# Kernel tuning notes

Measured on AMD Instinct MI355X. Metric: run time of the kernel, lower is better.

## Reference

```python
import jax, jax.numpy as jnp
import numpy as np

N_FLOWS, N_LINKS, L, P, D = 50000, 5000, 8, 80, 16
ITERS = 12
# (mean, scale) applied as (x - mean) * scale, matching the TF code
MS_FIELDS = ['flow_traffic', 'flow_packets', 'flow_pkts_per_burst', 'flow_bitrate_per_burst',
             'flow_packet_size', 'flow_p90PktSize', 'rate', 'flow_ipg_mean', 'ibg',
             'flow_ipg_var', 'link_capacity']
MS = {f: (0.1, 2.0) for f in MS_FIELDS}


def _gru(h, x, Wk, Wr, b):
    # Keras GRUCell (reset_after=True): bias has shape [2, 3D]
    a = x @ Wk + b[0]
    g = h @ Wr + b[1]
    az, ar, ah = jnp.split(a, 3, axis=-1)
    gz, gr, gh = jnp.split(g, 3, axis=-1)
    z = jax.nn.sigmoid(az + gz)
    r = jax.nn.sigmoid(ar + gr)
    return z * h + (1.0 - z) * jnp.tanh(ah + r * gh)


def setup_inputs() -> dict:
    key = jax.random.key(0)
    ks = jax.random.split(key, 48)
    u = lambda i, shape: jax.random.uniform(ks[i], shape, jnp.float32)
    w = lambda i, shape: (jax.random.normal(ks[i], shape, jnp.float32) * 0.3)
    inp = {
        'flow_traffic': u(0, (N_FLOWS, 1)),
        'flow_packets': u(1, (N_FLOWS, 1)),
        'max_link_load': jnp.ones((1, 1), jnp.float32),
        'flow_pkts_per_burst': u(2, (N_FLOWS, 1)),
        'flow_bitrate_per_burst': u(3, (N_FLOWS, 1)),
        'flow_packet_size': u(4, (N_FLOWS, 1)),
        'flow_type': u(5, (N_FLOWS, 2)),
        'flow_ipg_mean': u(6, (N_FLOWS, 1)),
        'ibg': u(7, (N_FLOWS, 1)),
        'flow_p90PktSize': u(8, (N_FLOWS, 1)),
        'rate': u(9, (N_FLOWS, 1)),
        'flow_ipg_var': u(10, (N_FLOWS, 1)),
        'link_capacity': u(11, (N_LINKS, 1)) + 0.5,  # keep capacities away from 0
        # params
        'fe_W1': w(12, (13, D)), 'fe_b1': jnp.zeros((D,), jnp.float32),
        'fe_W2': w(13, (D, D)), 'fe_b2': jnp.zeros((D,), jnp.float32),
        'le_W1': w(14, (3, D)), 'le_b1': jnp.zeros((D,), jnp.float32),
        'le_W2': w(15, (D, D)), 'le_b2': jnp.zeros((D,), jnp.float32),
        'att_W': w(16, (D, D)), 'att_b': jnp.zeros((D,), jnp.float32),
        'pgru_Wk': w(17, (D, 3 * D)), 'pgru_Wr': w(18, (D, 3 * D)),
        'pgru_b': jnp.zeros((2, 3 * D), jnp.float32),
        'lgru_Wk': w(19, (D, 3 * D)), 'lgru_Wr': w(20, (D, 3 * D)),
        'lgru_b': jnp.zeros((2, 3 * D), jnp.float32),
        'ro_W1': w(21, (D, D // 2)), 'ro_b1': jnp.zeros((D // 2,), jnp.float32),
        'ro_W2': w(22, (D // 2, D // 4)), 'ro_b2': jnp.zeros((D // 4,), jnp.float32),
        'ro_W3': w(23, (D // 4, 1)), 'ro_b3': jnp.zeros((1,), jnp.float32),
        # integer graph structure
        'flow_length': jax.random.randint(ks[24], (N_FLOWS,), 0, 1000, jnp.int32),
        'link_to_path': jax.random.randint(ks[25], (N_FLOWS, L), 0, N_LINKS, jnp.int32),
        'path_to_link': jnp.stack([
            jax.random.randint(ks[26], (N_LINKS, P), 0, N_FLOWS, jnp.int32),
            jax.random.randint(ks[27], (N_LINKS, P), 0, L + 1, jnp.int32)], axis=-1),
    }
    return inp


def reference(flow_traffic, flow_packets, max_link_load, flow_pkts_per_burst,
              flow_bitrate_per_burst, flow_packet_size, flow_type, flow_ipg_mean,
              ibg, flow_p90PktSize, rate, flow_ipg_var, link_capacity,
              fe_W1, fe_b1, fe_W2, fe_b2, le_W1, le_b1, le_W2, le_b2,
              att_W, att_b, pgru_Wk, pgru_Wr, pgru_b, lgru_Wk, lgru_Wr, lgru_b,
              ro_W1, ro_b1, ro_W2, ro_b2, ro_W3, ro_b3,
              flow_length, link_to_path, path_to_link):
    nrm = lambda x, f: (x - MS[f][0]) * MS[f][1]
    flow_idx = path_to_link[:, :, 0]   # [M, P]
    pos_idx = path_to_link[:, :, 1]    # [M, P]

    # link load from gathered flow traffic
    path_gather_traffic = flow_traffic[flow_idx]                 # [M, P, 1]
    load = path_gather_traffic.sum(axis=1) / (link_capacity * 1e9)
    normal_load = load / jnp.squeeze(max_link_load)

    flow_feats = jnp.concatenate([
        nrm(flow_traffic, 'flow_traffic'), nrm(flow_packets, 'flow_packets'),
        nrm(ibg, 'ibg'), nrm(rate, 'rate'), nrm(flow_p90PktSize, 'flow_p90PktSize'),
        nrm(flow_packet_size, 'flow_packet_size'),
        nrm(flow_bitrate_per_burst, 'flow_bitrate_per_burst'),
        nrm(flow_ipg_mean, 'flow_ipg_mean'), nrm(flow_ipg_var, 'flow_ipg_var'),
        nrm(flow_pkts_per_burst, 'flow_pkts_per_burst'),
        flow_length.astype(jnp.float32)[:, None], flow_type], axis=1)     # [N, 13]
    path_state = jax.nn.selu(jax.nn.selu(flow_feats @ fe_W1 + fe_b1) @ fe_W2 + fe_b2)

    link_feats = jnp.concatenate([nrm(link_capacity, 'link_capacity'), load, normal_load], axis=1)
    link_state = jax.nn.selu(jax.nn.selu(link_feats @ le_W1 + le_b1) @ le_W2 + le_b2)

    def rnn_step(h, x):
        h2 = _gru(h, x, pgru_Wk, pgru_Wr, pgru_b)
        return h2, h2

    path_state_sequence = None
    for _ in range(ITERS):
        link_gather = link_state[link_to_path]                   # [N, L, D]
        prev_path_state = path_state
        path_state, seq = jax.lax.scan(rnn_step, prev_path_state,
                                       jnp.swapaxes(link_gather, 0, 1))
        seq = jnp.swapaxes(seq, 0, 1)                            # [N, L, D]
        path_state_sequence = jnp.concatenate([prev_path_state[:, None], seq], axis=1)
        path_gather = path_state_sequence[flow_idx, pos_idx]     # [M, P, D]
        att = jax.nn.leaky_relu(path_gather @ att_W + att_b, negative_slope=0.01)
        score = jax.nn.softmax(att, axis=-1)                     # softmax over feature dim (K.softmax default)
        path_sum = (score * path_gather).sum(axis=1)             # [M, D]
        link_state = _gru(link_state, path_sum, lgru_Wk, lgru_Wr, lgru_b)

    h = jax.nn.selu(path_state_sequence[:, 1:] @ ro_W1 + ro_b1)
    h = jax.nn.selu(h @ ro_W2 + ro_b2)
    occupancy = jax.nn.softplus(h @ ro_W3 + ro_b3)               # [N, L, 1]
    capacity_gather = link_capacity[link_to_path]                # [N, L, 1]
    queue_delay = (occupancy / capacity_gather).sum(axis=1)      # [N, 1]
    return queue_delay
```

## Files before the change

kernel.cpp:

```cpp
#include <hip/hip_runtime.h>
#include <hip/hip_bf16.h>

#define N_FLOWS 50000
#define N_LINKS 5000
#define LPATH 8
#define PLINK 80
#define DIM 16
#define ITERS 12

typedef __attribute__((ext_vector_type(4))) float f32x4;
typedef __attribute__((ext_vector_type(8))) short bf16x8;

#define L2E 1.4426950408889634f
#define NL2E (-1.4426950408889634f)
#define P2L2E 2.8853900817779268f

#define SWZ(x, pat) __int_as_float(__builtin_amdgcn_ds_swizzle(__float_as_int(x), (pat)))

template <int CTRL>
__device__ __forceinline__ float dppmov_(float x) {
    return __int_as_float(__builtin_amdgcn_update_dpp(
        0, __float_as_int(x), CTRL, 0xF, 0xF, true));
}
#define ROR1 0x121
#define ROR2 0x122
#define ROR4 0x124
#define ROR8 0x128

__device__ __forceinline__ float rcp_(float x) { return __builtin_amdgcn_rcpf(x); }
__device__ __forceinline__ float exp2_(float x) { return __builtin_amdgcn_exp2f(x); }
__device__ __forceinline__ float sigmoid2_(float s) { return rcp_(1.f + exp2_(s)); }
__device__ __forceinline__ float tanh2_(float s) { return 1.f - 2.f * rcp_(1.f + exp2_(s)); }
__device__ __forceinline__ float selu_(float x) {
    const float sc = 1.0507009873554805f, al = 1.6732632423543772f;
    return x > 0.f ? sc * x : sc * al * expm1f(x);
}
__device__ __forceinline__ float softplus_(float x) {
    return fmaxf(x, 0.f) + log1pf(__expf(-fabsf(x)));
}
__device__ __forceinline__ ushort f2bf_(float x) {
    unsigned u = __float_as_uint(x);
    u += 0x7fffu + ((u >> 16) & 1u);
    return (ushort)(u >> 16);
}
__device__ __forceinline__ float bf2f_(ushort h) {
    return __uint_as_float(((unsigned)h) << 16);
}

__global__ __launch_bounds__(256) void k_prep(
    const float* __restrict__ pWr, const float* __restrict__ attW,
    const float* __restrict__ lWk, const float* __restrict__ lWr,
    const float* __restrict__ pWk,
    ushort* __restrict__ wfrag, float* __restrict__ lWk_t,
    float* __restrict__ lWr_t, float* __restrict__ pWk_t) {
    int i = blockIdx.x * 256 + threadIdx.x;
    if (i < 768) {
        int t = i;
        int j = t / 48, r = t % 48;
        float sc = (r / 16) == 2 ? P2L2E : NL2E;
        lWk_t[t] = lWk[(r % 16) * 48 + (r / 16) * 16 + j] * sc;
    } else if (i < 1536) {
        int t = i - 768;
        int j = t / 48, r = t % 48;
        float sc = (r / 16) == 2 ? P2L2E : NL2E;
        lWr_t[t] = lWr[(r % 16) * 48 + (r / 16) * 16 + j] * sc;
    } else if (i < 2304) {
        int t = i - 1536;
        pWk_t[t] = pWk[(t % 16) * 48 + (t / 16)];
    } else if (i < 6400) {
        int t = i - 2304;
        int frag = t >> 9;
        int s = t & 511;
        int lane = s >> 3;
        int e = s & 7;
        int gate = frag >> 1;
        int isLo = frag & 1;
        int n = lane & 15;
        int k = ((lane >> 4) * 8 + e) & 15;
        float raw;
        if (gate < 3) {
            float sc = gate == 2 ? P2L2E : NL2E;
            raw = pWr[k * 48 + gate * 16 + n] * sc;
        } else {
            raw = attW[k * 16 + n] * L2E;
        }
        ushort hi = f2bf_(raw);
        wfrag[t] = isLo ? f2bf_(raw - bf2f_(hi)) : hi;
    }
}

__global__ __launch_bounds__(256) void k_load(const int* __restrict__ p2l,
                                              const float* __restrict__ flow_traffic,
                                              const float* __restrict__ link_capacity,
                                              float* __restrict__ load) {
    int wave = (blockIdx.x * 256 + threadIdx.x) >> 6;
    int lane = threadIdx.x & 63;
    if (wave >= N_LINKS) return;
    float s = 0.f;
    for (int p = lane; p < PLINK; p += 64) {
        int flow = p2l[(wave * PLINK + p) * 2];
        s += flow_traffic[flow];
    }
#pragma unroll
    for (int off = 32; off; off >>= 1) s += __shfl_xor(s, off, 64);
    if (lane == 0) load[wave] = s / (link_capacity[wave] * 1e9f);
}

__global__ __launch_bounds__(256) void k_flow_init(
    const float* __restrict__ flow_traffic, const float* __restrict__ flow_packets,
    const float* __restrict__ ibg, const float* __restrict__ rate,
    const float* __restrict__ p90, const float* __restrict__ pkt_size,
    const float* __restrict__ bitrate_pb, const float* __restrict__ ipg_mean,
    const float* __restrict__ ipg_var, const float* __restrict__ pkts_pb,
    const int* __restrict__ flow_length, const float* __restrict__ flow_type,
    const float* __restrict__ W1, const float* __restrict__ b1,
    const float* __restrict__ W2, const float* __restrict__ b2,
    float* __restrict__ path_state) {
    int f = blockIdx.x * 256 + threadIdx.x;
    if (f >= N_FLOWS) return;
    float feats[13];
    feats[0] = (flow_traffic[f] - 0.1f) * 2.f;
    feats[1] = (flow_packets[f] - 0.1f) * 2.f;
    feats[2] = (ibg[f] - 0.1f) * 2.f;
    feats[3] = (rate[f] - 0.1f) * 2.f;
    feats[4] = (p90[f] - 0.1f) * 2.f;
    feats[5] = (pkt_size[f] - 0.1f) * 2.f;
    feats[6] = (bitrate_pb[f] - 0.1f) * 2.f;
    feats[7] = (ipg_mean[f] - 0.1f) * 2.f;
    feats[8] = (ipg_var[f] - 0.1f) * 2.f;
    feats[9] = (pkts_pb[f] - 0.1f) * 2.f;
    feats[10] = (float)flow_length[f];
    feats[11] = flow_type[f * 2 + 0];
    feats[12] = flow_type[f * 2 + 1];
    float h1[DIM];
#pragma unroll
    for (int j = 0; j < DIM; ++j) {
        float a = b1[j];
#pragma unroll
        for (int k = 0; k < 13; ++k) a = fmaf(feats[k], W1[k * DIM + j], a);
        h1[j] = selu_(a);
    }
#pragma unroll
    for (int j = 0; j < DIM; ++j) {
        float a = b2[j];
#pragma unroll
        for (int k = 0; k < DIM; ++k) a = fmaf(h1[k], W2[k * DIM + j], a);
        path_state[f * DIM + j] = selu_(a);
    }
}

__global__ __launch_bounds__(256) void k_link_init(
    const float* __restrict__ link_capacity, const float* __restrict__ load,
    const float* __restrict__ max_link_load,
    const float* __restrict__ W1, const float* __restrict__ b1,
    const float* __restrict__ W2, const float* __restrict__ b2,
    const float* __restrict__ pWk, const float* __restrict__ pb,
    float* __restrict__ link_state, float* __restrict__ xform) {
    int l = blockIdx.x * 256 + threadIdx.x;
    if (l >= N_LINKS) return;
    float feats[3];
    feats[0] = (link_capacity[l] - 0.1f) * 2.f;
    feats[1] = load[l];
    feats[2] = load[l] / max_link_load[0];
    float h1[DIM];
#pragma unroll
    for (int j = 0; j < DIM; ++j) {
        float a = b1[j];
#pragma unroll
        for (int k = 0; k < 3; ++k) a = fmaf(feats[k], W1[k * DIM + j], a);
        h1[j] = selu_(a);
    }
    float h2[DIM];
#pragma unroll
    for (int j = 0; j < DIM; ++j) {
        float a = b2[j];
#pragma unroll
        for (int k = 0; k < DIM; ++k) a = fmaf(h1[k], W2[k * DIM + j], a);
        h2[j] = selu_(a);
        link_state[l * DIM + j] = h2[j];
    }
#pragma unroll
    for (int c = 0; c < 3 * DIM; ++c) {
        float a = (c < 32) ? (pb[c] + pb[48 + c]) : pb[c];
#pragma unroll
        for (int k = 0; k < DIM; ++k) a = fmaf(h2[k], pWk[k * 48 + c], a);
        float sc = (c < 32) ? NL2E : P2L2E;
        xform[l * 64 + (c & 15) * 4 + (c >> 4)] = a * sc;
    }
}

template <bool LAST>
__global__ __launch_bounds__(256) void k_flow_pass(
    const int* __restrict__ l2p, const float* __restrict__ xform,
    float* __restrict__ path_state, float* __restrict__ sv,
    const ushort* __restrict__ wfrag, const float* __restrict__ b,
    const float* __restrict__ attB) {
    __shared__ __align__(16) ushort hx[4][16][40];
    __shared__ int lnk[4][16][8];
    int tid = threadIdx.x;
    int wid = tid >> 6, lane = tid & 63;
    int g = lane >> 4, j = lane & 15;
    int fbase = blockIdx.x * 64 + wid * 16;
    {
        int lf = lane >> 2;
        int off = (lane & 3) * 2;
        int fc = fbase + lf; if (fc >= N_FLOWS) fc = N_FLOWS - 1;
        int2 v = *(const int2*)(l2p + fc * LPATH + off);
        *(int2*)&lnk[wid][lf][off] = v;
    }
    bf16x8 WzH = *(const bf16x8*)(wfrag + (0 * 512 + lane * 8));
    bf16x8 WzL = *(const bf16x8*)(wfrag + (1 * 512 + lane * 8));
    bf16x8 WrH = *(const bf16x8*)(wfrag + (2 * 512 + lane * 8));
    bf16x8 WrL = *(const bf16x8*)(wfrag + (3 * 512 + lane * 8));
    bf16x8 WhH = *(const bf16x8*)(wfrag + (4 * 512 + lane * 8));
    bf16x8 WhL = *(const bf16x8*)(wfrag + (5 * 512 + lane * 8));
    bf16x8 WaH = *(const bf16x8*)(wfrag + (6 * 512 + lane * 8));
    bf16x8 WaL = *(const bf16x8*)(wfrag + (7 * 512 + lane * 8));
    float bh = P2L2E * b[80 + j];
    float ab = L2E * attB[j];
    f32x4 bhv = {bh, bh, bh, bh};
    f32x4 abv = {ab, ab, ab, ab};
    f32x4 zero = {0.f, 0.f, 0.f, 0.f};
    int fr[4];
    f32x4 hC;
#pragma unroll
    for (int r = 0; r < 4; ++r) {
        fr[r] = fbase + g * 4 + r;
        int fc = fr[r] < N_FLOWS ? fr[r] : N_FLOWS - 1;
        hC[r] = path_state[fc * DIM + j];
    }
#pragma unroll
    for (int p = 0; p <= LPATH; ++p) {
        bf16x8 A = {};
        if (!LAST || p < LPATH) {
#pragma unroll
            for (int r = 0; r < 4; ++r) {
                ushort hi = f2bf_(hC[r]);
                hx[wid][g * 4 + r][j] = hi;
                hx[wid][g * 4 + r][16 + j] = f2bf_(hC[r] - bf2f_(hi));
            }
            A = *(const bf16x8*)&hx[wid][j][g * 8];
        }
        if constexpr (!LAST) {
            f32x4 att = __builtin_amdgcn_mfma_f32_16x16x32_bf16(A, WaH, abv, 0, 0, 0);
            att = __builtin_amdgcn_mfma_f32_16x16x32_bf16(A, WaL, att, 0, 0, 0);
#pragma unroll
            for (int r = 0; r < 4; ++r) {
                float a = att[r];
                a = a > 0.f ? a : 0.01f * a;
                float m = a;
                m = fmaxf(m, dppmov_<ROR1>(m));
                m = fmaxf(m, dppmov_<ROR2>(m));
                m = fmaxf(m, dppmov_<ROR4>(m));
                m = fmaxf(m, dppmov_<ROR8>(m));
                float e = exp2_(a - m);
                float s = e;
                s += dppmov_<ROR1>(s);
                s += dppmov_<ROR2>(s);
                s += dppmov_<ROR4>(s);
                s += dppmov_<ROR8>(s);
                if (fr[r] < N_FLOWS)
                    sv[p * (N_FLOWS * DIM) + fr[r] * DIM + j] = e * rcp_(s) * hC[r];
            }
        } else {
            if (p > 0) {
#pragma unroll
                for (int r = 0; r < 4; ++r)
                    if (fr[r] < N_FLOWS)
                        sv[p * (N_FLOWS * DIM) + fr[r] * DIM + j] = hC[r];
            }
        }
        if (p < LPATH) {
            f32x4 Gz = __builtin_amdgcn_mfma_f32_16x16x32_bf16(A, WzH, zero, 0, 0, 0);
            Gz = __builtin_amdgcn_mfma_f32_16x16x32_bf16(A, WzL, Gz, 0, 0, 0);
            f32x4 Gr = __builtin_amdgcn_mfma_f32_16x16x32_bf16(A, WrH, zero, 0, 0, 0);
            Gr = __builtin_amdgcn_mfma_f32_16x16x32_bf16(A, WrL, Gr, 0, 0, 0);
            f32x4 Gh = __builtin_amdgcn_mfma_f32_16x16x32_bf16(A, WhH, bhv, 0, 0, 0);
            Gh = __builtin_amdgcn_mfma_f32_16x16x32_bf16(A, WhL, Gh, 0, 0, 0);
#pragma unroll
            for (int r = 0; r < 4; ++r) {
                int link = lnk[wid][g * 4 + r][p];
                f32x4 xq = *(const f32x4*)(xform + link * 64 + j * 4);
                float z = sigmoid2_(xq[0] + Gz[r]);
                float rr = sigmoid2_(xq[1] + Gr[r]);
                float cand = tanh2_(fmaf(rr, Gh[r], xq[2]));
                hC[r] = fmaf(z, hC[r] - cand, cand);
            }
        }
    }
    if constexpr (!LAST) {
#pragma unroll
        for (int r = 0; r < 4; ++r)
            if (fr[r] < N_FLOWS) path_state[fr[r] * DIM + j] = hC[r];
    }
}

__global__ __launch_bounds__(256, 4) void k_link_pass(
    const int* __restrict__ p2l, const float* __restrict__ sv,
    float* __restrict__ link_state,
    const float* __restrict__ lWk_t, const float* __restrict__ lWr_t,
    const float* __restrict__ b,
    const float* __restrict__ pWk_t, const float* __restrict__ pb,
    float* __restrict__ xform) {
    __shared__ float xb_[4][16];
    __shared__ float hb_[4][16];
    int tid = threadIdx.x;
    int li = tid >> 6;
    int lane = tid & 63;
    int sl = lane >> 4, j = lane & 15;
    int link = blockIdx.x * 4 + li;
    float ps = 0.f;
#pragma unroll 4
    for (int i = 0; i < PLINK / 4; ++i) {
        int p = sl + 4 * i;
        int2 fp = ((const int2*)p2l)[link * PLINK + p];
        ps += sv[fp.y * (N_FLOWS * DIM) + fp.x * DIM + j];
    }
    ps += __shfl_xor(ps, 16, 64);
    ps += __shfl_xor(ps, 32, 64);
    float h = link_state[link * DIM + j];
    if (sl == 0) { xb_[li][j] = ps; hb_[li][j] = h; }
    float xv[16], hv[16];
#pragma unroll
    for (int q = 0; q < 4; ++q) {
        f32x4 x4 = ((const f32x4*)xb_[li])[q];
        f32x4 h4 = ((const f32x4*)hb_[li])[q];
#pragma unroll
        for (int e = 0; e < 4; ++e) { xv[q * 4 + e] = x4[e]; hv[q * 4 + e] = h4[e]; }
    }
    float az = NL2E * b[j], ar = NL2E * b[16 + j], ah = P2L2E * b[32 + j];
    float gz = NL2E * b[48 + j], gr = NL2E * b[64 + j], gh = P2L2E * b[80 + j];
    const float* kz = lWk_t + j * 48;
    const float* rz = lWr_t + j * 48;
#pragma unroll
    for (int k = 0; k < 16; ++k) {
        az = fmaf(xv[k], kz[k], az);
        ar = fmaf(xv[k], kz[16 + k], ar);
        ah = fmaf(xv[k], kz[32 + k], ah);
        gz = fmaf(hv[k], rz[k], gz);
        gr = fmaf(hv[k], rz[16 + k], gr);
        gh = fmaf(hv[k], rz[32 + k], gh);
    }
    float z = sigmoid2_(az + gz);
    float r = sigmoid2_(ar + gr);
    float cand = tanh2_(fmaf(r, gh, ah));
    float hn = fmaf(z, h - cand, cand);
    if (sl == 0) {
        link_state[link * DIM + j] = hn;
        hb_[li][j] = hn;
    }
    float nv[16];
#pragma unroll
    for (int q = 0; q < 4; ++q) {
        f32x4 n4 = ((const f32x4*)hb_[li])[q];
#pragma unroll
        for (int e = 0; e < 4; ++e) nv[q * 4 + e] = n4[e];
    }
    int c = lane;
    if (c < 48) {
        const float* pw = pWk_t + c * 16;
        float a = (c < 32) ? (pb[c] + pb[48 + c]) : pb[c];
#pragma unroll
        for (int k = 0; k < 16; ++k) a = fmaf(nv[k], pw[k], a);
        float sc = (c < 32) ? NL2E : P2L2E;
        xform[link * 64 + (c & 15) * 4 + (c >> 4)] = a * sc;
    }
}

__global__ __launch_bounds__(256) void k_readout(
    const float* __restrict__ sv, const int* __restrict__ l2p,
    const float* __restrict__ link_capacity,
    const float* __restrict__ W1, const float* __restrict__ b1,
    const float* __restrict__ W2, const float* __restrict__ b2,
    const float* __restrict__ W3, const float* __restrict__ b3,
    float* __restrict__ out) {
    int tid = blockIdx.x * 256 + threadIdx.x;
    int f = tid >> 3;
    int t = tid & 7;
    if (f >= N_FLOWS) return;
    const float* s = sv + (t + 1) * (N_FLOWS * DIM) + f * DIM;
    float h1[8];
#pragma unroll
    for (int m_ = 0; m_ < 8; ++m_) {
        float a = b1[m_];
#pragma unroll
        for (int k = 0; k < 16; ++k) a = fmaf(s[k], W1[k * 8 + m_], a);
        h1[m_] = selu_(a);
    }
    float h2[4];
#pragma unroll
    for (int q = 0; q < 4; ++q) {
        float a = b2[q];
#pragma unroll
        for (int m_ = 0; m_ < 8; ++m_) a = fmaf(h1[m_], W2[m_ * 4 + q], a);
        h2[q] = selu_(a);
    }
    float o = b3[0];
#pragma unroll
    for (int q = 0; q < 4; ++q) o = fmaf(h2[q], W3[q], o);
    o = softplus_(o);
    int link = l2p[f * LPATH + t];
    float v = o * rcp_(link_capacity[link]);
    v += SWZ(v, 0x041F);
    v += SWZ(v, 0x081F);
    v += SWZ(v, 0x101F);
    if (t == 0) out[f] = v;
}

extern "C" void kernel_launch(void* const* d_in, const int* in_sizes, int n_in,
                              void* d_out, int out_size, void* d_ws, size_t ws_size,
                              hipStream_t stream) {
    const float* flow_traffic = (const float*)d_in[0];
    const float* flow_packets = (const float*)d_in[1];
    const float* max_link_load = (const float*)d_in[2];
    const float* flow_pkts_per_burst = (const float*)d_in[3];
    const float* flow_bitrate_per_burst = (const float*)d_in[4];
    const float* flow_packet_size = (const float*)d_in[5];
    const float* flow_type = (const float*)d_in[6];
    const float* flow_ipg_mean = (const float*)d_in[7];
    const float* ibg = (const float*)d_in[8];
    const float* flow_p90 = (const float*)d_in[9];
    const float* rate = (const float*)d_in[10];
    const float* flow_ipg_var = (const float*)d_in[11];
    const float* link_capacity = (const float*)d_in[12];
    const float* fe_W1 = (const float*)d_in[13];
    const float* fe_b1 = (const float*)d_in[14];
    const float* fe_W2 = (const float*)d_in[15];
    const float* fe_b2 = (const float*)d_in[16];
    const float* le_W1 = (const float*)d_in[17];
    const float* le_b1 = (const float*)d_in[18];
    const float* le_W2 = (const float*)d_in[19];
    const float* le_b2 = (const float*)d_in[20];
    const float* att_W = (const float*)d_in[21];
    const float* att_b = (const float*)d_in[22];
    const float* pgru_Wk = (const float*)d_in[23];
    const float* pgru_Wr = (const float*)d_in[24];
    const float* pgru_b = (const float*)d_in[25];
    const float* lgru_Wk = (const float*)d_in[26];
    const float* lgru_Wr = (const float*)d_in[27];
    const float* lgru_b = (const float*)d_in[28];
    const float* ro_W1 = (const float*)d_in[29];
    const float* ro_b1 = (const float*)d_in[30];
    const float* ro_W2 = (const float*)d_in[31];
    const float* ro_b2 = (const float*)d_in[32];
    const float* ro_W3 = (const float*)d_in[33];
    const float* ro_b3 = (const float*)d_in[34];
    const int* flow_length = (const int*)d_in[35];
    const int* l2p = (const int*)d_in[36];
    const int* p2l = (const int*)d_in[37];

    float* ws = (float*)d_ws;
    float* path_state = ws;
    float* link_state = ws + 800000;
    float* sv = ws + 880000;
    float* load = ws + 8080000;
    float* xform = ws + 8085000;
    ushort* wfrag = (ushort*)(ws + 8405000);
    float* lWk_t = ws + 8407048;
    float* lWr_t = ws + 8407816;
    float* pWk_t = ws + 8408584;
    if (ws_size < (size_t)8409352 * 4) return;

    k_prep<<<25, 256, 0, stream>>>(pgru_Wr, att_W, lgru_Wk, lgru_Wr, pgru_Wk,
                                   wfrag, lWk_t, lWr_t, pWk_t);
    k_load<<<(N_LINKS * 64 + 255) / 256, 256, 0, stream>>>(p2l, flow_traffic,
                                                           link_capacity, load);
    k_flow_init<<<(N_FLOWS + 255) / 256, 256, 0, stream>>>(
        flow_traffic, flow_packets, ibg, rate, flow_p90, flow_packet_size,
        flow_bitrate_per_burst, flow_ipg_mean, flow_ipg_var, flow_pkts_per_burst,
        flow_length, flow_type, fe_W1, fe_b1, fe_W2, fe_b2, path_state);
    k_link_init<<<(N_LINKS + 255) / 256, 256, 0, stream>>>(
        link_capacity, load, max_link_load, le_W1, le_b1, le_W2, le_b2,
        pgru_Wk, pgru_b, link_state, xform);

    int fp_grid = (N_FLOWS + 63) / 64;
    for (int it = 0; it < ITERS - 1; ++it) {
        k_flow_pass<false><<<fp_grid, 256, 0, stream>>>(
            l2p, xform, path_state, sv, wfrag, pgru_b, att_b);
        k_link_pass<<<N_LINKS / 4, 256, 0, stream>>>(
            p2l, sv, link_state, lWk_t, lWr_t, lgru_b, pWk_t, pgru_b, xform);
    }
    k_flow_pass<true><<<fp_grid, 256, 0, stream>>>(
        l2p, xform, path_state, sv, wfrag, pgru_b, att_b);
    k_readout<<<(N_FLOWS * 8 + 255) / 256, 256, 0, stream>>>(
        sv, l2p, link_capacity, ro_W1, ro_b1, ro_W2, ro_b2, ro_W3, ro_b3,
        (float*)d_out);
}
```

Before: 461.4 us.

## Fuse readout into final flow pass and prefetch next-hop link transforms

```diff
diff --git a/kernel.cpp b/kernel.cpp
--- a/kernel.cpp
+++ b/kernel.cpp
@@ -16,6 +16,7 @@
 #define P2L2E 2.8853900817779268f
 
 #define SWZ(x, pat) __int_as_float(__builtin_amdgcn_ds_swizzle(__float_as_int(x), (pat)))
+#define MFMA16(A, B, C) __builtin_amdgcn_mfma_f32_16x16x32_bf16((A), (B), (C), 0, 0, 0)
 
 template <int CTRL>
 __device__ __forceinline__ float dppmov_(float x) {
@@ -194,9 +195,15 @@
     const int* __restrict__ l2p, const float* __restrict__ xform,
     float* __restrict__ path_state, float* __restrict__ sv,
     const ushort* __restrict__ wfrag, const float* __restrict__ b,
-    const float* __restrict__ attB) {
+    const float* __restrict__ attB,
+    const float* __restrict__ link_capacity,
+    const float* __restrict__ roW1, const float* __restrict__ rob1,
+    const float* __restrict__ roW2, const float* __restrict__ rob2,
+    const float* __restrict__ roW3, const float* __restrict__ rob3,
+    float* __restrict__ out) {
     __shared__ __align__(16) ushort hx[4][16][40];
     __shared__ int lnk[4][16][8];
+    __shared__ float shist[LAST ? 4 : 1][16][LPATH][17];
     int tid = threadIdx.x;
     int wid = tid >> 6, lane = tid & 63;
     int g = lane >> 4, j = lane & 15;
@@ -205,30 +212,27 @@
         int lf = lane >> 2;
         int off = (lane & 3) * 2;
         int fc = fbase + lf; if (fc >= N_FLOWS) fc = N_FLOWS - 1;
-        int2 v = *(const int2*)(l2p + fc * LPATH + off);
-        *(int2*)&lnk[wid][lf][off] = v;
-    }
-    bf16x8 WzH = *(const bf16x8*)(wfrag + (0 * 512 + lane * 8));
-    bf16x8 WzL = *(const bf16x8*)(wfrag + (1 * 512 + lane * 8));
-    bf16x8 WrH = *(const bf16x8*)(wfrag + (2 * 512 + lane * 8));
-    bf16x8 WrL = *(const bf16x8*)(wfrag + (3 * 512 + lane * 8));
-    bf16x8 WhH = *(const bf16x8*)(wfrag + (4 * 512 + lane * 8));
-    bf16x8 WhL = *(const bf16x8*)(wfrag + (5 * 512 + lane * 8));
-    bf16x8 WaH = *(const bf16x8*)(wfrag + (6 * 512 + lane * 8));
-    bf16x8 WaL = *(const bf16x8*)(wfrag + (7 * 512 + lane * 8));
+        *(int2*)&lnk[wid][lf][off] = *(const int2*)(l2p + fc * LPATH + off);
+    }
+    bf16x8 Wf[8];
+#pragma unroll
+    for (int q = 0; q < 8; ++q) Wf[q] = *(const bf16x8*)(wfrag + q * 512 + lane * 8);
     float bh = P2L2E * b[80 + j];
     float ab = L2E * attB[j];
     f32x4 bhv = {bh, bh, bh, bh};
     f32x4 abv = {ab, ab, ab, ab};
     f32x4 zero = {0.f, 0.f, 0.f, 0.f};
-    int fr[4];
+    int fr0 = fbase + g * 4;
     f32x4 hC;
 #pragma unroll
     for (int r = 0; r < 4; ++r) {
-        fr[r] = fbase + g * 4 + r;
-        int fc = fr[r] < N_FLOWS ? fr[r] : N_FLOWS - 1;
+        int fc = fr0 + r; if (fc >= N_FLOWS) fc = N_FLOWS - 1;
         hC[r] = path_state[fc * DIM + j];
     }
+    f32x4 xq[4];
+#pragma unroll
+    for (int r = 0; r < 4; ++r)
+        xq[r] = *(const f32x4*)(xform + lnk[wid][g * 4 + r][0] * 64 + j * 4);
 #pragma unroll
     for (int p = 0; p <= LPATH; ++p) {
         bf16x8 A = {};
@@ -242,8 +246,8 @@
             A = *(const bf16x8*)&hx[wid][j][g * 8];
         }
         if constexpr (!LAST) {
-            f32x4 att = __builtin_amdgcn_mfma_f32_16x16x32_bf16(A, WaH, abv, 0, 0, 0);
-            att = __builtin_amdgcn_mfma_f32_16x16x32_bf16(A, WaL, att, 0, 0, 0);
+            f32x4 att = MFMA16(A, Wf[6], abv);
+            att = MFMA16(A, Wf[7], att);
 #pragma unroll
             for (int r = 0; r < 4; ++r) {
                 float a = att[r];
@@ -259,39 +263,87 @@
                 s += dppmov_<ROR2>(s);
                 s += dppmov_<ROR4>(s);
                 s += dppmov_<ROR8>(s);
-                if (fr[r] < N_FLOWS)
-                    sv[p * (N_FLOWS * DIM) + fr[r] * DIM + j] = e * rcp_(s) * hC[r];
+                if (fr0 + r < N_FLOWS)
+                    sv[p * (N_FLOWS * DIM) + (fr0 + r) * DIM + j] =
+                        e * rcp_(s) * hC[r];
             }
         } else {
             if (p > 0) {
 #pragma unroll
                 for (int r = 0; r < 4; ++r)
-                    if (fr[r] < N_FLOWS)
-                        sv[p * (N_FLOWS * DIM) + fr[r] * DIM + j] = hC[r];
+                    shist[wid][g * 4 + r][p - 1][j] = hC[r];
             }
         }
         if (p < LPATH) {
-            f32x4 Gz = __builtin_amdgcn_mfma_f32_16x16x32_bf16(A, WzH, zero, 0, 0, 0);
-            Gz = __builtin_amdgcn_mfma_f32_16x16x32_bf16(A, WzL, Gz, 0, 0, 0);
-            f32x4 Gr = __builtin_amdgcn_mfma_f32_16x16x32_bf16(A, WrH, zero, 0, 0, 0);
-            Gr = __builtin_amdgcn_mfma_f32_16x16x32_bf16(A, WrL, Gr, 0, 0, 0);
-            f32x4 Gh = __builtin_amdgcn_mfma_f32_16x16x32_bf16(A, WhH, bhv, 0, 0, 0);
-            Gh = __builtin_amdgcn_mfma_f32_16x16x32_bf16(A, WhL, Gh, 0, 0, 0);
+            f32x4 nxq[4];
+#pragma unroll
+            for (int r = 0; r < 4; ++r) nxq[r] = xq[r];
+            if (p + 1 < LPATH) {
+#pragma unroll
+                for (int r = 0; r < 4; ++r)
+                    nxq[r] = *(const f32x4*)(xform +
+                                             lnk[wid][g * 4 + r][p + 1] * 64 +
+                                             j * 4);
+            }
+            f32x4 Gz = MFMA16(A, Wf[0], zero);
+            Gz = MFMA16(A, Wf[1], Gz);
+            f32x4 Gr = MFMA16(A, Wf[2], zero);
+            Gr = MFMA16(A, Wf[3], Gr);
+            f32x4 Gh = MFMA16(A, Wf[4], bhv);
+            Gh = MFMA16(A, Wf[5], Gh);
 #pragma unroll
             for (int r = 0; r < 4; ++r) {
-                int link = lnk[wid][g * 4 + r][p];
-                f32x4 xq = *(const f32x4*)(xform + link * 64 + j * 4);
-                float z = sigmoid2_(xq[0] + Gz[r]);
-                float rr = sigmoid2_(xq[1] + Gr[r]);
-                float cand = tanh2_(fmaf(rr, Gh[r], xq[2]));
+                float z = sigmoid2_(xq[r][0] + Gz[r]);
+                float rr = sigmoid2_(xq[r][1] + Gr[r]);
+                float cand = tanh2_(fmaf(rr, Gh[r], xq[r][2]));
                 hC[r] = fmaf(z, hC[r] - cand, cand);
             }
+#pragma unroll
+            for (int r = 0; r < 4; ++r) xq[r] = nxq[r];
         }
     }
     if constexpr (!LAST) {
 #pragma unroll
         for (int r = 0; r < 4; ++r)
-            if (fr[r] < N_FLOWS) path_state[fr[r] * DIM + j] = hC[r];
+            if (fr0 + r < N_FLOWS) path_state[(fr0 + r) * DIM + j] = hC[r];
+    } else {
+        __syncthreads();
+        int fl = tid >> 2;
+        int q = tid & 3;
+        int fwid = fl >> 4, f16 = fl & 15;
+        int fg = blockIdx.x * 64 + fl;
+        float acc = 0.f;
+#pragma unroll
+        for (int tt = 0; tt < 2; ++tt) {
+            int t = q + tt * 4;
+            const float* s = shist[fwid][f16][t];
+            float h1[8];
+#pragma unroll
+            for (int m_ = 0; m_ < 8; ++m_) {
+                float a = rob1[m_];
+#pragma unroll
+                for (int k = 0; k < 16; ++k) a = fmaf(s[k], roW1[k * 8 + m_], a);
+                h1[m_] = selu_(a);
+            }
+            float h2[4];
+#pragma unroll
+            for (int qq = 0; qq < 4; ++qq) {
+                float a = rob2[qq];
+#pragma unroll
+                for (int m_ = 0; m_ < 8; ++m_)
+                    a = fmaf(h1[m_], roW2[m_ * 4 + qq], a);
+                h2[qq] = selu_(a);
+            }
+            float o = rob3[0];
+#pragma unroll
+            for (int qq = 0; qq < 4; ++qq) o = fmaf(h2[qq], roW3[qq], o);
+            o = softplus_(o);
+            int link = lnk[fwid][f16][t];
+            acc += o * rcp_(link_capacity[link]);
+        }
+        acc += SWZ(acc, 0x041F);
+        acc += SWZ(acc, 0x081F);
+        if (q == 0 && fg < N_FLOWS) out[fg] = acc;
     }
 }
 
@@ -365,46 +417,6 @@
         float sc = (c < 32) ? NL2E : P2L2E;
         xform[link * 64 + (c & 15) * 4 + (c >> 4)] = a * sc;
     }
-}
-
-__global__ __launch_bounds__(256) void k_readout(
-    const float* __restrict__ sv, const int* __restrict__ l2p,
-    const float* __restrict__ link_capacity,
-    const float* __restrict__ W1, const float* __restrict__ b1,
-    const float* __restrict__ W2, const float* __restrict__ b2,
-    const float* __restrict__ W3, const float* __restrict__ b3,
-    float* __restrict__ out) {
-    int tid = blockIdx.x * 256 + threadIdx.x;
-    int f = tid >> 3;
-    int t = tid & 7;
-    if (f >= N_FLOWS) return;
-    const float* s = sv + (t + 1) * (N_FLOWS * DIM) + f * DIM;
-    float h1[8];
-#pragma unroll
-    for (int m_ = 0; m_ < 8; ++m_) {
-        float a = b1[m_];
-#pragma unroll
-        for (int k = 0; k < 16; ++k) a = fmaf(s[k], W1[k * 8 + m_], a);
-        h1[m_] = selu_(a);
-    }
-    float h2[4];
-#pragma unroll
-    for (int q = 0; q < 4; ++q) {
-        float a = b2[q];
-#pragma unroll
-        for (int m_ = 0; m_ < 8; ++m_) a = fmaf(h1[m_], W2[m_ * 4 + q], a);
-        h2[q] = selu_(a);
-    }
-    float o = b3[0];
-#pragma unroll
-    for (int q = 0; q < 4; ++q) o = fmaf(h2[q], W3[q], o);
-    o = softplus_(o);
-    int link = l2p[f * LPATH + t];
-    float v = o * rcp_(link_capacity[link]);
-    v += SWZ(v, 0x041F);
-    v += SWZ(v, 0x081F);
-    v += SWZ(v, 0x101F);
-    if (t == 0) out[f] = v;
 }
 
 extern "C" void kernel_launch(void* const* d_in, const int* in_sizes, int n_in,
@@ -476,13 +488,14 @@
     int fp_grid = (N_FLOWS + 63) / 64;
     for (int it = 0; it < ITERS - 1; ++it) {
         k_flow_pass<false><<<fp_grid, 256, 0, stream>>>(
-            l2p, xform, path_state, sv, wfrag, pgru_b, att_b);
+            l2p, xform, path_state, sv, wfrag, pgru_b, att_b,
+            nullptr, nullptr, nullptr, nullptr, nullptr, nullptr, nullptr,
+            nullptr);
         k_link_pass<<<N_LINKS / 4, 256, 0, stream>>>(
             p2l, sv, link_state, lWk_t, lWr_t, lgru_b, pWk_t, pgru_b, xform);
     }
     k_flow_pass<true><<<fp_grid, 256, 0, stream>>>(
-        l2p, xform, path_state, sv, wfrag, pgru_b, att_b);
-    k_readout<<<(N_FLOWS * 8 + 255) / 256, 256, 0, stream>>>(
-        sv, l2p, link_capacity, ro_W1, ro_b1, ro_W2, ro_b2, ro_W3, ro_b3,
+        l2p, xform, path_state, sv, wfrag, pgru_b, att_b,
+        link_capacity, ro_W1, ro_b1, ro_W2, ro_b2, ro_W3, ro_b3,
         (float*)d_out);
 }
```

Result: no change. 469.6 us (+1.8%).
